# Kernel optimization log

Hardware: AMD Instinct MI355X
Metric: run time of the kernel (lower is better)

## Reference

```python
import jax, jax.numpy as jnp
from jax import lax
import numpy as np

B, S, I, H, L = 128, 256, 512, 768, 2  # batch, seq, input, hidden, layers


def _lstm_dir(x_seq, Wx, bx, Wh, bh, h0, c0):
    """Run one LSTM direction over x_seq [B,S,D]. Gate order f,i,g,o (as torch.chunk)."""
    xg = jnp.einsum('bsd,dg->bsg', x_seq, Wx) + bx  # precompute input projections [B,S,4H]

    def step(carry, xg_t):
        h, c = carry
        gates = xg_t + h @ Wh + bh
        f, i, g, o = jnp.split(gates, 4, axis=-1)
        c = jax.nn.sigmoid(f) * c + jax.nn.sigmoid(i) * jnp.tanh(g)
        h = jax.nn.sigmoid(o) * jnp.tanh(c)
        return (h, c), h

    (h, c), hs = lax.scan(step, (h0, c0), jnp.swapaxes(xg, 0, 1))  # scan over time
    return jnp.swapaxes(hs, 0, 1), h, c  # outputs [B,S,H], final h, c


def _mk_params(key, in_dim, hid):
    k1, k2 = jax.random.split(key)
    s_x = 1.0 / np.sqrt(in_dim)
    s_h = 1.0 / np.sqrt(hid)
    Wx = jax.random.uniform(k1, (in_dim, 4 * hid), jnp.float32, -s_x, s_x)
    bx = jnp.zeros((4 * hid,), jnp.float32)
    Wh = jax.random.uniform(k2, (hid, 4 * hid), jnp.float32, -s_h, s_h)
    bh = jnp.zeros((4 * hid,), jnp.float32)
    return Wx, bx, Wh, bh


def setup_inputs() -> dict:
    key = jax.random.key(0)
    ks = jax.random.split(key, 5)
    x = jax.random.normal(ks[0], (B, S, I), jnp.float32)
    out = {'x': x}
    names = [('f0', I), ('f1', H), ('b0', I), ('b1', H)]
    for k, (tag, in_dim) in zip(ks[1:], names):
        Wx, bx, Wh, bh = _mk_params(k, in_dim, H)
        out[f'Wx_{tag}'] = Wx
        out[f'bx_{tag}'] = bx
        out[f'Wh_{tag}'] = Wh
        out[f'bh_{tag}'] = bh
    return out


def reference(x, Wx_f0, bx_f0, Wh_f0, bh_f0, Wx_f1, bx_f1, Wh_f1, bh_f1,
              Wx_b0, bx_b0, Wh_b0, bh_b0, Wx_b1, bx_b1, Wh_b1, bh_b1):
    b = x.shape[0]
    z = jnp.zeros((b, H), x.dtype)
    fwd_params = [(Wx_f0, bx_f0, Wh_f0, bh_f0), (Wx_f1, bx_f1, Wh_f1, bh_f1)]
    bwd_params = [(Wx_b0, bx_b0, Wh_b0, bh_b0), (Wx_b1, bx_b1, Wh_b1, bh_b1)]

    inp_f = x
    inp_b = jnp.flip(x, axis=1)  # backward direction consumes reversed sequence
    h_f, c_f, h_b, c_b = [], [], [], []
    for layer in range(L):
        inp_f, hf, cf = _lstm_dir(inp_f, *fwd_params[layer], z, z)
        h_f.append(hf); c_f.append(cf)
        inp_b, hb, cb = _lstm_dir(inp_b, *bwd_params[layer], z, z)
        h_b.append(hb); c_b.append(cb)

    output = jnp.concatenate([inp_f, jnp.flip(inp_b, axis=1)], axis=-1)  # [B,S,2H]
    h_n = jnp.stack(h_f + h_b, axis=0)  # [2L,B,H], forward layers then backward
    c_n = jnp.stack(c_f + c_b, axis=0)
    return output, h_n, c_n
```

## Files before the change

kernel.cpp:

```cpp
#include <hip/hip_runtime.h>

#define BATCH 128
#define SEQ   256
#define IDIM  512
#define HDIM  768
#define G4    3072
#define BK    32

typedef __bf16 bf16;
typedef __bf16 bf16x8 __attribute__((ext_vector_type(8)));
typedef float  f32x4  __attribute__((ext_vector_type(4)));

__device__ __forceinline__ float sigf(float x){ return 1.f/(1.f + __expf(-x)); }
__device__ __forceinline__ float tanhf_(float x){ return 1.f - 2.f/(1.f + __expf(2.f*x)); }

__device__ __forceinline__ void gll16(const bf16* g, bf16* l){
  __builtin_amdgcn_global_load_lds(
      (const __attribute__((address_space(1))) void*)g,
      (__attribute__((address_space(3))) void*)l, 16, 0, 0);
}


__global__ void convert_x_k(const float* __restrict__ x, bf16* __restrict__ xb){
  long i = ((long)blockIdx.x*256 + threadIdx.x)*8;
  float4 a = *(const float4*)(x+i);
  float4 b = *(const float4*)(x+i+4);
  bf16x8 o;
  o[0]=(bf16)a.x; o[1]=(bf16)a.y; o[2]=(bf16)a.z; o[3]=(bf16)a.w;
  o[4]=(bf16)b.x; o[5]=(bf16)b.y; o[6]=(bf16)b.z; o[7]=(bf16)b.w;
  *(bf16x8*)(xb+i) = o;
}

__global__ void build_wt_k(const float* __restrict__ wx, const float* __restrict__ wh,
                           bf16* __restrict__ wt, int k0, int kc){
  int idx = blockIdx.x*256 + threadIdx.x;
  int c = idx / kc;
  int k = idx - c*kc;
  int g = (c >> 4) & 3;
  int j = ((c >> 6) << 4) | (c & 15);
  int oc = g*HDIM + j;
  float v = (k < k0) ? wx[(long)k*G4 + oc] : wh[(long)(k-k0)*G4 + oc];
  wt[idx] = (bf16)v;
}

__global__ void build_bias_k(const float* __restrict__ bx, const float* __restrict__ bh,
                             float* __restrict__ bc){
  int c = blockIdx.x*256 + threadIdx.x;
  int g = (c >> 4) & 3;
  int j = ((c >> 6) << 4) | (c & 15);
  int oc = g*HDIM + j;
  bc[c] = bx[oc] + bh[oc];
}


struct CellP {
  const bf16* seg0;
  const bf16* seg1;
  const bf16* wt;
  const float* bias;
  float* cbuf;
  bf16*  hout;
  float* out;
  float* hn;
  float* cn;
  int s0stride, k0, kc, active;
};
struct StepArgs { CellP cell[4]; };

__launch_bounds__(256, 2)
__global__ void lstm_step_k(StepArgs args){
  const CellP p = args.cell[blockIdx.x / 48];
  if (!p.active) return;
  int r = blockIdx.x % 48;
  int mtile = r / 24, ntile = r % 24;
  int tid = threadIdx.x;
  int lane = tid & 63, w = tid >> 6;
  int wm = w >> 1, wn = w & 1;
  int l15 = lane & 15, q = lane >> 4;

  __shared__ __align__(16) bf16 sA[4][64*BK];
  __shared__ __align__(16) bf16 sB[4][128*BK];

  f32x4 acc[2][4] = {};

  int rl  = lane >> 2;
  int lch = (lane & 3) ^ ((lane >> 3) & 3);

  int ra = w*16 + rl;
  int ga = mtile*64 + ra;
  const bf16* a0 = p.seg0 + (long)ga * p.s0stride + lch*8;
  const bf16* a1 = p.seg1 + (long)ga * HDIM + lch*8 - p.k0;

  long ncol0 = (long)ntile*128;
  const bf16* b0p = p.wt + (ncol0 + w*16     + rl) * (long)p.kc + lch*8;
  const bf16* b1p = p.wt + (ncol0 + (w+4)*16 + rl) * (long)p.kc + lch*8;

  bf16* sAw  = &sA[0][0] + w*512;
  bf16* sBw0 = &sB[0][0] + w*512;
  bf16* sBw1 = &sB[0][0] + (w+4)*512;

  int nk = p.kc / BK;
  int k0 = p.k0;

#pragma unroll
  for (int pb = 0; pb < 3; ++pb){
    const bf16* as = (pb*BK < k0) ? (a0 + pb*BK) : (a1 + pb*BK);
    gll16(as,          sAw  + pb*(64*BK));
    gll16(b0p + pb*BK, sBw0 + pb*(128*BK));
    gll16(b1p + pb*BK, sBw1 + pb*(128*BK));
  }

  int psel = (q ^ ((l15 >> 1) & 3)) * 8;

  for (int kb = 0; kb < nk; ++kb){
    int rem = nk - 1 - kb;
    if (rem >= 2)      asm volatile("s_waitcnt vmcnt(6)" ::: "memory");
    else if (rem == 1) asm volatile("s_waitcnt vmcnt(3)" ::: "memory");
    else               asm volatile("s_waitcnt vmcnt(0)" ::: "memory");
    __builtin_amdgcn_s_barrier();
    __builtin_amdgcn_sched_barrier(0);

    int nb = kb + 3;
    if (nb < nk){
      int buf = nb & 3;
      const bf16* as = (nb*BK < k0) ? (a0 + nb*BK) : (a1 + nb*BK);
      gll16(as,          sAw  + buf*(64*BK));
      gll16(b0p + nb*BK, sBw0 + buf*(128*BK));
      gll16(b1p + nb*BK, sBw1 + buf*(128*BK));
    }

    const bf16* A  = sA[kb & 3];
    const bf16* Bm = sB[kb & 3];
    bf16x8 af[2], bfr[4];
#pragma unroll
    for (int mi = 0; mi < 2; ++mi)
      af[mi] = *(const bf16x8*)(A + (wm*32 + mi*16 + l15)*BK + psel);
#pragma unroll
    for (int ni = 0; ni < 4; ++ni)
      bfr[ni] = *(const bf16x8*)(Bm + (wn*64 + ni*16 + l15)*BK + psel);
#pragma unroll
    for (int mi = 0; mi < 2; ++mi)
#pragma unroll
      for (int ni = 0; ni < 4; ++ni)
        acc[mi][ni] = __builtin_amdgcn_mfma_f32_16x16x32_bf16(af[mi], bfr[ni], acc[mi][ni], 0, 0, 0);
    __builtin_amdgcn_sched_barrier(0);
  }

  int colb = ntile*128 + wn*64;
  int j = ((colb >> 6) << 4) | l15;
  float bias4[4];
#pragma unroll
  for (int ni=0; ni<4; ++ni) bias4[ni] = p.bias[colb + ni*16 + l15];

#pragma unroll
  for (int mi=0; mi<2; ++mi){
    int b0 = mtile*64 + wm*32 + mi*16 + q*4;
#pragma unroll
    for (int rg=0; rg<4; ++rg){
      int b = b0 + rg;
      float fg = acc[mi][0][rg] + bias4[0];
      float ig = acc[mi][1][rg] + bias4[1];
      float gg = acc[mi][2][rg] + bias4[2];
      float og = acc[mi][3][rg] + bias4[3];
      float co = p.cbuf[b*HDIM + j];
      float cn = sigf(fg)*co + sigf(ig)*tanhf_(gg);
      float h  = sigf(og)*tanhf_(cn);
      p.cbuf[b*HDIM + j] = cn;
      p.hout[b*HDIM + j] = (bf16)h;
      if (p.out) p.out[(long)b*(SEQ*2*HDIM) + j] = h;
      if (p.hn){ p.hn[b*HDIM + j] = h; p.cn[b*HDIM + j] = cn; }
    }
  }
}


extern "C" void kernel_launch(void* const* d_in, const int* in_sizes, int n_in,
                              void* d_out, int out_size, void* d_ws, size_t ws_size,
                              hipStream_t stream){
  (void)in_sizes; (void)n_in; (void)out_size; (void)ws_size;
  const float* x = (const float*)d_in[0];
  const float* Wx[4]; const float* bxp[4]; const float* Whp[4]; const float* bhp[4];
  for (int t=0; t<4; ++t){
    Wx[t]  = (const float*)d_in[1 + 4*t];
    bxp[t] = (const float*)d_in[2 + 4*t];
    Whp[t] = (const float*)d_in[3 + 4*t];
    bhp[t] = (const float*)d_in[4 + 4*t];
  }
  const int tag[4] = {0, 2, 1, 3};
  const int k0c[4] = {IDIM, IDIM, HDIM, HDIM};
  const int kcc[4] = {IDIM+HDIM, IDIM+HDIM, 2*HDIM, 2*HDIM};

  char* ws = (char*)d_ws;
  size_t off = 0;
  auto take = [&](size_t bytes)->char*{ char* pp = ws + off; off += (bytes + 255) & ~(size_t)255; return pp; };

  bf16* xb = (bf16*)take((size_t)BATCH*SEQ*IDIM*2);
  bf16* wt[4];    for (int c=0;c<4;++c) wt[c]   = (bf16*)take((size_t)G4*kcc[c]*2);
  float* bias[4]; for (int c=0;c<4;++c) bias[c] = (float*)take((size_t)G4*4);
  bf16* hseq[4];  for (int c=0;c<4;++c) hseq[c] = (bf16*)take((size_t)SEQ*BATCH*HDIM*2);
  bf16* zeros = (bf16*)take((size_t)BATCH*HDIM*2);
  float* cbuf[4]; for (int c=0;c<4;++c) cbuf[c] = (float*)take((size_t)BATCH*HDIM*4);

  size_t zlen = (size_t)BATCH*HDIM*2 + 4*(size_t)BATCH*HDIM*4;
  hipMemsetAsync(zeros, 0, zlen, stream);

  convert_x_k<<<dim3((BATCH*SEQ*IDIM)/(8*256)), dim3(256), 0, stream>>>(x, xb);
  for (int c=0;c<4;++c)
    build_wt_k<<<dim3((G4*kcc[c])/256), dim3(256), 0, stream>>>(Wx[tag[c]], Whp[tag[c]], wt[c], k0c[c], kcc[c]);
  for (int c=0;c<4;++c)
    build_bias_k<<<dim3(G4/256), dim3(256), 0, stream>>>(bxp[tag[c]], bhp[tag[c]], bias[c]);

  float* outF = (float*)d_out;
  float* hnF  = outF + (size_t)BATCH*SEQ*2*HDIM;
  float* cnF  = hnF + (size_t)4*BATCH*HDIM;
  const int hnidx[4] = {0, 2, 1, 3};
  const size_t BH = (size_t)BATCH*HDIM;

  for (int kk=0; kk<=SEQ; ++kk){
    StepArgs A;
    for (int c=0; c<2; ++c){
      CellP& P = A.cell[c];
      int t = (kk < SEQ) ? kk : 0;
      P.active = (kk < SEQ);
      int ts = (c==0) ? t : (SEQ-1-t);
      P.seg0 = xb + (size_t)ts*IDIM;
      P.s0stride = SEQ*IDIM;
      P.k0 = k0c[c]; P.kc = kcc[c];
      P.seg1 = (t==0) ? zeros : (hseq[c] + (size_t)(t-1)*BH);
      P.wt = wt[c]; P.bias = bias[c]; P.cbuf = cbuf[c];
      P.hout = hseq[c] + (size_t)t*BH;
      P.out = nullptr;
      if (P.active && t == SEQ-1){ P.hn = hnF + hnidx[c]*BH; P.cn = cnF + hnidx[c]*BH; }
      else { P.hn = nullptr; P.cn = nullptr; }
    }
    for (int c=2; c<4; ++c){
      CellP& P = A.cell[c];
      int t = (kk >= 1) ? (kk-1) : 0;
      P.active = (kk >= 1);
      P.seg0 = hseq[c-2] + (size_t)t*BH;
      P.s0stride = HDIM;
      P.k0 = k0c[c]; P.kc = kcc[c];
      P.seg1 = (t==0) ? zeros : (hseq[c] + (size_t)(t-1)*BH);
      P.wt = wt[c]; P.bias = bias[c]; P.cbuf = cbuf[c];
      P.hout = hseq[c] + (size_t)t*BH;
      P.out = (c==2) ? (outF + (size_t)t*2*HDIM)
                     : (outF + (size_t)(SEQ-1-t)*2*HDIM + HDIM);
      if (P.active && t == SEQ-1){ P.hn = hnF + hnidx[c]*BH; P.cn = cnF + hnidx[c]*BH; }
      else { P.hn = nullptr; P.cn = nullptr; }
    }
    lstm_step_k<<<dim3(192), dim3(256), 0, stream>>>(A);
  }
}
```

Baseline: 7.597 ms.

## Replace per-timestep launches with a persistent kernel using grid barriers

```diff
diff --git a/kernel.cpp b/kernel.cpp
--- a/kernel.cpp
+++ b/kernel.cpp
@@ -6,6 +6,9 @@
 #define HDIM  768
 #define G4    3072
 #define BK    32
+#define RING  8
+#define DEPTH 5
+#define NBLK  192
 
 typedef __bf16 bf16;
 typedef __bf16 bf16x8 __attribute__((ext_vector_type(8)));
@@ -53,123 +56,171 @@
 }
 
 
-struct CellP {
-  const bf16* seg0;
-  const bf16* seg1;
-  const bf16* wt;
-  const float* bias;
-  float* cbuf;
-  bf16*  hout;
-  float* out;
-  float* hn;
-  float* cn;
-  int s0stride, k0, kc, active;
+struct PArgs {
+  const bf16* xb;
+  const bf16* wt[4];
+  const float* bias[4];
+  bf16* hseq[4];
+  const bf16* zeros;
+  float* outF; float* hnF; float* cnF;
+  int* bcnt; int* bgen;
 };
-struct StepArgs { CellP cell[4]; };
-
-__launch_bounds__(256, 2)
-__global__ void lstm_step_k(StepArgs args){
-  const CellP p = args.cell[blockIdx.x / 48];
-  if (!p.active) return;
-  int r = blockIdx.x % 48;
-  int mtile = r / 24, ntile = r % 24;
-  int tid = threadIdx.x;
-  int lane = tid & 63, w = tid >> 6;
-  int wm = w >> 1, wn = w & 1;
-  int l15 = lane & 15, q = lane >> 4;
-
-  __shared__ __align__(16) bf16 sA[4][64*BK];
-  __shared__ __align__(16) bf16 sB[4][128*BK];
-
-  f32x4 acc[2][4] = {};
-
-  int rl  = lane >> 2;
-  int lch = (lane & 3) ^ ((lane >> 3) & 3);
-
-  int ra = w*16 + rl;
-  int ga = mtile*64 + ra;
-  const bf16* a0 = p.seg0 + (long)ga * p.s0stride + lch*8;
-  const bf16* a1 = p.seg1 + (long)ga * HDIM + lch*8 - p.k0;
-
-  long ncol0 = (long)ntile*128;
-  const bf16* b0p = p.wt + (ncol0 + w*16     + rl) * (long)p.kc + lch*8;
-  const bf16* b1p = p.wt + (ncol0 + (w+4)*16 + rl) * (long)p.kc + lch*8;
-
-  bf16* sAw  = &sA[0][0] + w*512;
-  bf16* sBw0 = &sB[0][0] + w*512;
-  bf16* sBw1 = &sB[0][0] + (w+4)*512;
-
-  int nk = p.kc / BK;
-  int k0 = p.k0;
-
-#pragma unroll
-  for (int pb = 0; pb < 3; ++pb){
-    const bf16* as = (pb*BK < k0) ? (a0 + pb*BK) : (a1 + pb*BK);
-    gll16(as,          sAw  + pb*(64*BK));
-    gll16(b0p + pb*BK, sBw0 + pb*(128*BK));
-    gll16(b1p + pb*BK, sBw1 + pb*(128*BK));
+
+__device__ __forceinline__ void grid_barrier(int* cnt, int* gen, int target){
+  __syncthreads();
+  if (threadIdx.x == 0){
+    __threadfence();
+    int v = __hip_atomic_fetch_add(cnt, 1, __ATOMIC_ACQ_REL, __HIP_MEMORY_SCOPE_AGENT);
+    if (v == NBLK-1){
+      __hip_atomic_store(cnt, 0, __ATOMIC_RELAXED, __HIP_MEMORY_SCOPE_AGENT);
+      __hip_atomic_store(gen, target, __ATOMIC_RELEASE, __HIP_MEMORY_SCOPE_AGENT);
+    } else {
+      while (__hip_atomic_load(gen, __ATOMIC_ACQUIRE, __HIP_MEMORY_SCOPE_AGENT) < target)
+        __builtin_amdgcn_s_sleep(1);
+    }
   }
-
-  int psel = (q ^ ((l15 >> 1) & 3)) * 8;
-
-  for (int kb = 0; kb < nk; ++kb){
-    int rem = nk - 1 - kb;
-    if (rem >= 2)      asm volatile("s_waitcnt vmcnt(6)" ::: "memory");
-    else if (rem == 1) asm volatile("s_waitcnt vmcnt(3)" ::: "memory");
-    else               asm volatile("s_waitcnt vmcnt(0)" ::: "memory");
-    __builtin_amdgcn_s_barrier();
-    __builtin_amdgcn_sched_barrier(0);
-
-    int nb = kb + 3;
-    if (nb < nk){
-      int buf = nb & 3;
-      const bf16* as = (nb*BK < k0) ? (a0 + nb*BK) : (a1 + nb*BK);
-      gll16(as,          sAw  + buf*(64*BK));
-      gll16(b0p + nb*BK, sBw0 + buf*(128*BK));
-      gll16(b1p + nb*BK, sBw1 + buf*(128*BK));
+  __syncthreads();
+}
+
+__launch_bounds__(256, 1)
+__global__ void lstm_persist_k(PArgs a){
+  const int c = blockIdx.x / 48;
+  const int r = blockIdx.x % 48;
+  const int mtile = r / 24, ntile = r % 24;
+  const int tid = threadIdx.x;
+  const int lane = tid & 63, wv = tid >> 6;
+  const int wm = wv >> 1, wn = wv & 1;
+  const int l15 = lane & 15, q = lane >> 4;
+
+  const int k0 = (c < 2) ? IDIM : HDIM;
+  const int kc = (c < 2) ? (IDIM + HDIM) : (2*HDIM);
+  const int nk = kc / BK;
+
+  __shared__ __align__(16) bf16 sA[RING][64*BK];
+  __shared__ __align__(16) bf16 sB[RING][128*BK];
+
+  const int rl  = lane >> 2;
+  const int lch = (lane & 3) ^ ((lane >> 3) & 3);
+  const int ra  = wv*16 + rl;
+  const int ga  = mtile*64 + ra;
+
+  const long ncol0 = (long)ntile*128;
+  const bf16* wtc = a.wt[c];
+  const bf16* b0p = wtc + (ncol0 + wv*16     + rl) * (long)kc + lch*8;
+  const bf16* b1p = wtc + (ncol0 + (wv+4)*16 + rl) * (long)kc + lch*8;
+
+  bf16* sAw  = &sA[0][0] + wv*512;
+  bf16* sBw0 = &sB[0][0] + wv*512;
+  bf16* sBw1 = &sB[0][0] + (wv+4)*512;
+
+  const int psel = (q ^ ((l15 >> 1) & 3)) * 8;
+
+  const int colb = ntile*128 + wn*64;
+  const int j = ((colb >> 6) << 4) | l15;
+  float bias4[4];
+#pragma unroll
+  for (int ni=0; ni<4; ++ni) bias4[ni] = a.bias[c][colb + ni*16 + l15];
+  const int hni = (c==0) ? 0 : (c==1) ? 2 : (c==2) ? 1 : 3;
+  const size_t BH = (size_t)BATCH*HDIM;
+  bf16* hseqc = a.hseq[c];
+
+  float creg[2][4] = {{0.f,0.f,0.f,0.f},{0.f,0.f,0.f,0.f}};
+
+  for (int kk = 0; kk <= SEQ; ++kk){
+    int active, t;
+    const bf16* seg0; long s0stride;
+    if (c < 2){
+      active = (kk < SEQ); t = active ? kk : 0;
+      int ts = (c==0) ? t : (SEQ-1-t);
+      seg0 = a.xb + (size_t)ts*IDIM; s0stride = (long)SEQ*IDIM;
+    } else {
+      active = (kk >= 1); t = active ? (kk-1) : 0;
+      seg0 = a.hseq[c-2] + (size_t)t*BH; s0stride = HDIM;
     }
 
-    const bf16* A  = sA[kb & 3];
-    const bf16* Bm = sB[kb & 3];
-    bf16x8 af[2], bfr[4];
-#pragma unroll
-    for (int mi = 0; mi < 2; ++mi)
-      af[mi] = *(const bf16x8*)(A + (wm*32 + mi*16 + l15)*BK + psel);
-#pragma unroll
-    for (int ni = 0; ni < 4; ++ni)
-      bfr[ni] = *(const bf16x8*)(Bm + (wn*64 + ni*16 + l15)*BK + psel);
-#pragma unroll
-    for (int mi = 0; mi < 2; ++mi)
-#pragma unroll
-      for (int ni = 0; ni < 4; ++ni)
-        acc[mi][ni] = __builtin_amdgcn_mfma_f32_16x16x32_bf16(af[mi], bfr[ni], acc[mi][ni], 0, 0, 0);
-    __builtin_amdgcn_sched_barrier(0);
-  }
-
-  int colb = ntile*128 + wn*64;
-  int j = ((colb >> 6) << 4) | l15;
-  float bias4[4];
-#pragma unroll
-  for (int ni=0; ni<4; ++ni) bias4[ni] = p.bias[colb + ni*16 + l15];
-
-#pragma unroll
-  for (int mi=0; mi<2; ++mi){
-    int b0 = mtile*64 + wm*32 + mi*16 + q*4;
-#pragma unroll
-    for (int rg=0; rg<4; ++rg){
-      int b = b0 + rg;
-      float fg = acc[mi][0][rg] + bias4[0];
-      float ig = acc[mi][1][rg] + bias4[1];
-      float gg = acc[mi][2][rg] + bias4[2];
-      float og = acc[mi][3][rg] + bias4[3];
-      float co = p.cbuf[b*HDIM + j];
-      float cn = sigf(fg)*co + sigf(ig)*tanhf_(gg);
-      float h  = sigf(og)*tanhf_(cn);
-      p.cbuf[b*HDIM + j] = cn;
-      p.hout[b*HDIM + j] = (bf16)h;
-      if (p.out) p.out[(long)b*(SEQ*2*HDIM) + j] = h;
-      if (p.hn){ p.hn[b*HDIM + j] = h; p.cn[b*HDIM + j] = cn; }
+    if (active){
+      const bf16* seg1 = (t==0) ? a.zeros : (hseqc + (size_t)(t-1)*BH);
+      const bf16* a0 = seg0 + (long)ga * s0stride + lch*8;
+      const bf16* a1 = seg1 + (long)ga * HDIM + lch*8 - k0;
+
+      f32x4 acc[2][4] = {};
+
+#pragma unroll
+      for (int pb = 0; pb < DEPTH; ++pb){
+        const bf16* as = (pb*BK < k0) ? (a0 + pb*BK) : (a1 + pb*BK);
+        gll16(as,          sAw  + pb*(64*BK));
+        gll16(b0p + pb*BK, sBw0 + pb*(128*BK));
+        gll16(b1p + pb*BK, sBw1 + pb*(128*BK));
+      }
+
+      for (int kb = 0; kb < nk; ++kb){
+        int w_ = nk-1-kb;
+        if (w_ >= 4)      asm volatile("s_waitcnt vmcnt(12)" ::: "memory");
+        else if (w_ == 3) asm volatile("s_waitcnt vmcnt(9)"  ::: "memory");
+        else if (w_ == 2) asm volatile("s_waitcnt vmcnt(6)"  ::: "memory");
+        else if (w_ == 1) asm volatile("s_waitcnt vmcnt(3)"  ::: "memory");
+        else              asm volatile("s_waitcnt vmcnt(0)"  ::: "memory");
+        __builtin_amdgcn_s_barrier();
+        __builtin_amdgcn_sched_barrier(0);
+
+        int nb = kb + DEPTH;
+        if (nb < nk){
+          int buf = nb & (RING-1);
+          const bf16* as = (nb*BK < k0) ? (a0 + nb*BK) : (a1 + nb*BK);
+          gll16(as,          sAw  + buf*(64*BK));
+          gll16(b0p + nb*BK, sBw0 + buf*(128*BK));
+          gll16(b1p + nb*BK, sBw1 + buf*(128*BK));
+        }
+
+        const bf16* A  = sA[kb & (RING-1)];
+        const bf16* Bm = sB[kb & (RING-1)];
+        bf16x8 af[2], bfr[4];
+#pragma unroll
+        for (int mi = 0; mi < 2; ++mi)
+          af[mi] = *(const bf16x8*)(A + (wm*32 + mi*16 + l15)*BK + psel);
+#pragma unroll
+        for (int ni = 0; ni < 4; ++ni)
+          bfr[ni] = *(const bf16x8*)(Bm + (wn*64 + ni*16 + l15)*BK + psel);
+#pragma unroll
+        for (int mi = 0; mi < 2; ++mi)
+#pragma unroll
+          for (int ni = 0; ni < 4; ++ni)
+            acc[mi][ni] = __builtin_amdgcn_mfma_f32_16x16x32_bf16(af[mi], bfr[ni], acc[mi][ni], 0, 0, 0);
+        __builtin_amdgcn_sched_barrier(0);
+      }
+
+      float* op = nullptr;
+      if (c >= 2)
+        op = (c==2) ? (a.outF + (size_t)t*2*HDIM)
+                    : (a.outF + (size_t)(SEQ-1-t)*2*HDIM + HDIM);
+      bf16* hrow = hseqc + (size_t)t*BH;
+      const int last = (t == SEQ-1);
+
+#pragma unroll
+      for (int mi=0; mi<2; ++mi){
+        int b0 = mtile*64 + wm*32 + mi*16 + q*4;
+#pragma unroll
+        for (int rg=0; rg<4; ++rg){
+          int b = b0 + rg;
+          float fg = acc[mi][0][rg] + bias4[0];
+          float ig = acc[mi][1][rg] + bias4[1];
+          float gg = acc[mi][2][rg] + bias4[2];
+          float og = acc[mi][3][rg] + bias4[3];
+          float co = creg[mi][rg];
+          float cn = sigf(fg)*co + sigf(ig)*tanhf_(gg);
+          float h  = sigf(og)*tanhf_(cn);
+          creg[mi][rg] = cn;
+          hrow[b*HDIM + j] = (bf16)h;
+          if (op) op[(long)b*(SEQ*2*HDIM) + j] = h;
+          if (last){
+            a.hnF[hni*BH + b*HDIM + j] = h;
+            a.cnF[hni*BH + b*HDIM + j] = cn;
+          }
+        }
+      }
     }
+
+    if (kk < SEQ) grid_barrier(a.bcnt, a.bgen, kk+1);
   }
 }
 
@@ -199,10 +250,10 @@
   float* bias[4]; for (int c=0;c<4;++c) bias[c] = (float*)take((size_t)G4*4);
   bf16* hseq[4];  for (int c=0;c<4;++c) hseq[c] = (bf16*)take((size_t)SEQ*BATCH*HDIM*2);
   bf16* zeros = (bf16*)take((size_t)BATCH*HDIM*2);
-  float* cbuf[4]; for (int c=0;c<4;++c) cbuf[c] = (float*)take((size_t)BATCH*HDIM*4);
-
-  size_t zlen = (size_t)BATCH*HDIM*2 + 4*(size_t)BATCH*HDIM*4;
-  hipMemsetAsync(zeros, 0, zlen, stream);
+  int*  barp  = (int*)take(512);
+
+  size_t zlen = (size_t)BATCH*HDIM*2 + 512;
+  (void)hipMemsetAsync(zeros, 0, zlen, stream);
 
   convert_x_k<<<dim3((BATCH*SEQ*IDIM)/(8*256)), dim3(256), 0, stream>>>(x, xb);
   for (int c=0;c<4;++c)
@@ -213,41 +264,13 @@
   float* outF = (float*)d_out;
   float* hnF  = outF + (size_t)BATCH*SEQ*2*HDIM;
   float* cnF  = hnF + (size_t)4*BATCH*HDIM;
-  const int hnidx[4] = {0, 2, 1, 3};
-  const size_t BH = (size_t)BATCH*HDIM;
-
-  for (int kk=0; kk<=SEQ; ++kk){
-    StepArgs A;
-    for (int c=0; c<2; ++c){
-      CellP& P = A.cell[c];
-      int t = (kk < SEQ) ? kk : 0;
-      P.active = (kk < SEQ);
-      int ts = (c==0) ? t : (SEQ-1-t);
-      P.seg0 = xb + (size_t)ts*IDIM;
-      P.s0stride = SEQ*IDIM;
-      P.k0 = k0c[c]; P.kc = kcc[c];
-      P.seg1 = (t==0) ? zeros : (hseq[c] + (size_t)(t-1)*BH);
-      P.wt = wt[c]; P.bias = bias[c]; P.cbuf = cbuf[c];
-      P.hout = hseq[c] + (size_t)t*BH;
-      P.out = nullptr;
-      if (P.active && t == SEQ-1){ P.hn = hnF + hnidx[c]*BH; P.cn = cnF + hnidx[c]*BH; }
-      else { P.hn = nullptr; P.cn = nullptr; }
-    }
-    for (int c=2; c<4; ++c){
-      CellP& P = A.cell[c];
-      int t = (kk >= 1) ? (kk-1) : 0;
-      P.active = (kk >= 1);
-      P.seg0 = hseq[c-2] + (size_t)t*BH;
-      P.s0stride = HDIM;
-      P.k0 = k0c[c]; P.kc = kcc[c];
-      P.seg1 = (t==0) ? zeros : (hseq[c] + (size_t)(t-1)*BH);
-      P.wt = wt[c]; P.bias = bias[c]; P.cbuf = cbuf[c];
-      P.hout = hseq[c] + (size_t)t*BH;
-      P.out = (c==2) ? (outF + (size_t)t*2*HDIM)
-                     : (outF + (size_t)(SEQ-1-t)*2*HDIM + HDIM);
-      if (P.active && t == SEQ-1){ P.hn = hnF + hnidx[c]*BH; P.cn = cnF + hnidx[c]*BH; }
-      else { P.hn = nullptr; P.cn = nullptr; }
-    }
-    lstm_step_k<<<dim3(192), dim3(256), 0, stream>>>(A);
-  }
-}
+
+  PArgs A;
+  A.xb = xb;
+  for (int c=0;c<4;++c){ A.wt[c] = wt[c]; A.bias[c] = bias[c]; A.hseq[c] = hseq[c]; }
+  A.zeros = zeros;
+  A.outF = outF; A.hnF = hnF; A.cnF = cnF;
+  A.bcnt = barp; A.bgen = barp + 64;
+
+  lstm_persist_k<<<dim3(NBLK), dim3(256), 0, stream>>>(A);
+}
```

New measurement: 10.68 ms. +40.6%, slower.
